# Kernel optimization log

Measured on AMD Instinct MI355X. Metric: run time of the kernel, lower is better.

Reference implementation:

```python
import jax, jax.numpy as jnp
import numpy as np

HIDDEN_DIM = 64
VOCAB_SIZE = 64
NUM_SLOTS = 64
B, L = 256, 4096
EPS = 1e-5


def setup_inputs() -> dict:
    key = jax.random.key(0)
    ks = jax.random.split(key, 8)
    s = 0.02
    return {
        "seq": jax.random.randint(ks[0], (B, L), 0, VOCAB_SIZE),
        "embed": jax.random.normal(ks[1], (VOCAB_SIZE, HIDDEN_DIM), jnp.float32) * s,
        "W1": jax.random.normal(ks[2], (HIDDEN_DIM, 2 * HIDDEN_DIM), jnp.float32) * s,
        "b1": jnp.zeros((2 * HIDDEN_DIM,), jnp.float32),
        "W2": jax.random.normal(ks[3], (2 * HIDDEN_DIM, HIDDEN_DIM), jnp.float32) * s,
        "b2": jnp.zeros((HIDDEN_DIM,), jnp.float32),
        "gamma": jnp.ones((HIDDEN_DIM,), jnp.float32),
        "beta": jnp.zeros((HIDDEN_DIM,), jnp.float32),
        "Wq": jax.random.normal(ks[4], (HIDDEN_DIM, HIDDEN_DIM), jnp.float32) * s,
        "bq": jnp.zeros((HIDDEN_DIM,), jnp.float32),
        "Wo": jax.random.normal(ks[5], (HIDDEN_DIM, VOCAB_SIZE), jnp.float32) * s,
        "bo": jnp.zeros((VOCAB_SIZE,), jnp.float32),
    }


def reference(seq, embed, W1, b1, W2, b2, gamma, beta, Wq, bq, Wo, bo):
    # Encoder: embed -> FF residual -> LayerNorm
    e = embed[seq]                                   # [B, L, H]
    ff = jax.nn.relu(e @ W1 + b1) @ W2 + b2          # [B, L, H]
    h = e + ff
    mu = jnp.mean(h, axis=-1, keepdims=True)
    var = jnp.mean(jnp.square(h - mu), axis=-1, keepdims=True)
    hs = (h - mu) * jax.lax.rsqrt(var + EPS) * gamma + beta  # [B, L, H]

    # Top-k gating over content token norms
    content = hs[:, :-3, :]                          # [B, L-3, H]
    gate_scores = jnp.linalg.norm(content, axis=-1)  # [B, L-3]
    _, idx = jax.lax.top_k(gate_scores, NUM_SLOTS)   # [B, k], k == num_slots (L-3 >= k)
    slots = jnp.take_along_axis(content, idx[:, :, None], axis=1)  # [B, k, H]

    # Tiny single-query attention over gathered slots
    q = hs[:, -1, :] @ Wq + bq                       # [B, H]
    scores = jnp.einsum("bh,bkh->bk", q, slots) / jnp.sqrt(jnp.float32(HIDDEN_DIM))
    attn = jax.nn.softmax(scores, axis=-1)           # [B, k]
    ctx = jnp.einsum("bk,bkh->bh", attn, slots)      # [B, H]
    return ctx @ Wo + bo                             # [B, VOCAB]
```

## Files before the change

### kernel.cpp

```cpp
#include <hip/hip_runtime.h>
#include <math.h>

#define EPS 1e-5f


__global__ __launch_bounds__(256) void table_and_hist(
    const int* __restrict__ seq,
    const float* __restrict__ embed,
    const float* __restrict__ W1, const float* __restrict__ b1,
    const float* __restrict__ W2, const float* __restrict__ b2,
    const float* __restrict__ gamma, const float* __restrict__ beta,
    float* __restrict__ wsf, int* __restrict__ wsi_hist,
    int* __restrict__ wsi_tlast)
{
    const int tid = threadIdx.x;

    if (blockIdx.x < 64) {
        __shared__ float W1s[64][128];
        __shared__ float W2s[128][64];
        __shared__ float e[64];
        __shared__ float Up[2][128];
        __shared__ float U[128];
        __shared__ float Hp[4][64];

        const int t = blockIdx.x;

        #pragma unroll
        for (int i = 0; i < 8; ++i) {
            reinterpret_cast<float4*>(&W1s[0][0])[tid + 256 * i] =
                reinterpret_cast<const float4*>(W1)[tid + 256 * i];
            reinterpret_cast<float4*>(&W2s[0][0])[tid + 256 * i] =
                reinterpret_cast<const float4*>(W2)[tid + 256 * i];
        }
        if (tid < 64) e[tid] = embed[t * 64 + tid];
        __syncthreads();

        {
            int j = tid & 127, h = tid >> 7;
            int k0 = h << 5;
            float acc = 0.f;
            #pragma unroll 8
            for (int k = 0; k < 32; ++k)
                acc = fmaf(e[k0 + k], W1s[k0 + k][j], acc);
            Up[h][j] = acc;
        }
        __syncthreads();
        if (tid < 128) U[tid] = fmaxf(b1[tid] + Up[0][tid] + Up[1][tid], 0.f);
        __syncthreads();

        {
            int j = tid & 63, qd = tid >> 6;
            int k0 = qd << 5;
            float acc = 0.f;
            #pragma unroll 8
            for (int k = 0; k < 32; ++k)
                acc = fmaf(U[k0 + k], W2s[k0 + k][j], acc);
            Hp[qd][j] = acc;
        }
        __syncthreads();

        if (tid < 64) {
            float h = e[tid] + b2[tid] + Hp[0][tid] + Hp[1][tid] + Hp[2][tid] + Hp[3][tid];
            float s = h;
            #pragma unroll
            for (int off = 1; off < 64; off <<= 1) s += __shfl_xor(s, off);
            float mu = s * (1.f / 64.f);
            float d = h - mu;
            float v = d * d;
            #pragma unroll
            for (int off = 1; off < 64; off <<= 1) v += __shfl_xor(v, off);
            float rstd = rsqrtf(v * (1.f / 64.f) + EPS);
            float hs = d * rstd * gamma[tid] + beta[tid];
            wsf[t * 64 + tid] = hs;
            float ss = hs * hs;
            #pragma unroll
            for (int off = 1; off < 64; off <<= 1) ss += __shfl_xor(ss, off);
            if (tid == 0) wsf[4096 + t] = sqrtf(ss);
        }
    } else {
        __shared__ int hist[4][64];
        const int b = blockIdx.x - 64;
        const int wv = tid >> 6, ln = tid & 63;
        const int* row = seq + b * 4096;

        hist[wv][ln] = 0;
        __syncthreads();

        #pragma unroll
        for (int i = 0; i < 4; ++i) {
            int idx = tid + 256 * i;
            if (idx < 1023) {
                int4 v = reinterpret_cast<const int4*>(row)[idx];
                atomicAdd(&hist[wv][v.x], 1);
                atomicAdd(&hist[wv][v.y], 1);
                atomicAdd(&hist[wv][v.z], 1);
                atomicAdd(&hist[wv][v.w], 1);
            }
        }
        if (tid == 0) {
            atomicAdd(&hist[0][row[4092]], 1);
            wsi_tlast[b] = row[4095];
        }
        __syncthreads();

        if (tid < 64)
            wsi_hist[b * 64 + tid] =
                hist[0][tid] + hist[1][tid] + hist[2][tid] + hist[3][tid];
    }
}

__global__ __launch_bounds__(256) void slot_epilogue(
    const float* __restrict__ Wq, const float* __restrict__ bq,
    const float* __restrict__ Wo, const float* __restrict__ bo,
    const float* __restrict__ wsf, const int* __restrict__ wsi_hist,
    const int* __restrict__ wsi_tlast,
    float* __restrict__ out)
{
    __shared__ float HS[64][65];
    __shared__ float qv[64];

    const int tid = threadIdx.x;
    const int wv  = tid >> 6;
    const int ln  = tid & 63;
    const int b   = blockIdx.x;

    float wcol[64];
    float bias = 0.f, sc_r = 0.f;
    int h = 0, tl = 0;
    if (wv == 0) {
        #pragma unroll
        for (int k = 0; k < 64; ++k) wcol[k] = Wo[k * 64 + ln];
        bias = bo[ln];
        sc_r = wsf[4096 + ln];
        h    = wsi_hist[b * 64 + ln];
    } else if (wv == 1) {
        #pragma unroll
        for (int k = 0; k < 64; ++k) wcol[k] = Wq[k * 64 + ln];
        bias = bq[ln];
        tl   = wsi_tlast[b];
    }

    #pragma unroll
    for (int i = 0; i < 4; ++i) {
        int idx4 = tid + 256 * i;
        float4 v = reinterpret_cast<const float4*>(wsf)[idx4];
        int t  = idx4 >> 4;
        int j0 = (idx4 & 15) << 2;
        HS[t][j0] = v.x; HS[t][j0+1] = v.y; HS[t][j0+2] = v.z; HS[t][j0+3] = v.w;
    }
    __syncthreads();

    int cnt_i = 0;
    if (wv == 0) {
        float my = sc_r;
        int S = 0;
        for (int t2 = 0; t2 < 64; ++t2) {
            float s2 = __shfl(sc_r, t2);
            int   h2 = __shfl(h, t2);
            bool before = (s2 > my) || (s2 == my && t2 < ln);
            if (before) S += h2;
        }
        int rem = 64 - S;
        rem = rem < 0 ? 0 : rem;
        cnt_i = h < rem ? h : rem;
    } else if (wv == 1) {
        float acc = bias;
        #pragma unroll
        for (int k = 0; k < 64; ++k)
            acc = fmaf(HS[tl][k], wcol[k], acc);
        qv[ln] = acc;
    }
    __syncthreads();

    if (wv == 0) {
        float acc = 0.f;
        #pragma unroll 8
        for (int k = 0; k < 64; ++k)
            acc = fmaf(qv[k], HS[ln][k], acc);
        float logit = acc * 0.125f;
        float lm = (cnt_i > 0) ? logit : -1e30f;
        #pragma unroll
        for (int off = 1; off < 64; off <<= 1) lm = fmaxf(lm, __shfl_xor(lm, off));
        float wvv = (cnt_i > 0) ? (float)cnt_i * __expf(logit - lm) : 0.f;
        float z = wvv;
        #pragma unroll
        for (int off = 1; off < 64; off <<= 1) z += __shfl_xor(z, off);
        float w_reg = wvv / z;

        float cacc = 0.f;
        #pragma unroll 8
        for (int t2 = 0; t2 < 64; ++t2)
            cacc = fmaf(__shfl(w_reg, t2), HS[t2][ln], cacc);

        float oacc = bias;
        #pragma unroll
        for (int k = 0; k < 64; ++k)
            oacc = fmaf(__shfl(cacc, k), wcol[k], oacc);
        out[b * 64 + ln] = oacc;
    }
}

extern "C" void kernel_launch(void* const* d_in, const int* in_sizes, int n_in,
                              void* d_out, int out_size, void* d_ws, size_t ws_size,
                              hipStream_t stream) {
    const int*   seq   = (const int*)d_in[0];
    const float* embed = (const float*)d_in[1];
    const float* W1    = (const float*)d_in[2];
    const float* b1    = (const float*)d_in[3];
    const float* W2    = (const float*)d_in[4];
    const float* b2    = (const float*)d_in[5];
    const float* gamma = (const float*)d_in[6];
    const float* beta  = (const float*)d_in[7];
    const float* Wq    = (const float*)d_in[8];
    const float* bq    = (const float*)d_in[9];
    const float* Wo    = (const float*)d_in[10];
    const float* bo    = (const float*)d_in[11];
    float* out = (float*)d_out;
    float* wsf = (float*)d_ws;
    int*   wsi_hist  = (int*)(wsf + 4160);
    int*   wsi_tlast = wsi_hist + 256 * 64;
    (void)in_sizes; (void)n_in; (void)out_size; (void)ws_size;

    table_and_hist<<<320, 256, 0, stream>>>(seq, embed, W1, b1, W2, b2,
                                            gamma, beta, wsf, wsi_hist, wsi_tlast);
    slot_epilogue<<<256, 256, 0, stream>>>(Wq, bq, Wo, bo, wsf, wsi_hist,
                                           wsi_tlast, out);
}
```

Baseline: 16.94 us.

## Compute embedding table per wavefront with shuffles and widen histogram blocks

The encoder table is now computed one token per wavefront, eight tokens per 512-thread block. Each block reads W1/W2 straight from global memory and broadcasts activations with shuffles, where before every block staged both weight matrices into shared memory. The histogram blocks grow to 512 threads, issue both int4 loads before the barrier, and handle the tail token without a serial thread-0 path. The goal is to drop the large shared-memory staging and its barriers, at the cost of repeated global or L2 weight reads in the table blocks.

```diff
diff --git a/kernel.cpp b/kernel.cpp
--- a/kernel.cpp
+++ b/kernel.cpp
@@ -4,7 +4,7 @@
 #define EPS 1e-5f
 
 
-__global__ __launch_bounds__(256) void table_and_hist(
+__global__ __launch_bounds__(512) void table_hist(
     const int* __restrict__ seq,
     const float* __restrict__ embed,
     const float* __restrict__ W1, const float* __restrict__ b1,
@@ -14,98 +14,83 @@
     int* __restrict__ wsi_tlast)
 {
     const int tid = threadIdx.x;
-
-    if (blockIdx.x < 64) {
-        __shared__ float W1s[64][128];
-        __shared__ float W2s[128][64];
-        __shared__ float e[64];
-        __shared__ float Up[2][128];
-        __shared__ float U[128];
-        __shared__ float Hp[4][64];
-
-        const int t = blockIdx.x;
-
-        #pragma unroll
-        for (int i = 0; i < 8; ++i) {
-            reinterpret_cast<float4*>(&W1s[0][0])[tid + 256 * i] =
-                reinterpret_cast<const float4*>(W1)[tid + 256 * i];
-            reinterpret_cast<float4*>(&W2s[0][0])[tid + 256 * i] =
-                reinterpret_cast<const float4*>(W2)[tid + 256 * i];
-        }
-        if (tid < 64) e[tid] = embed[t * 64 + tid];
+    const int wv  = tid >> 6;
+    const int ln  = tid & 63;
+
+    if (blockIdx.x < 8) {
+        const int t = blockIdx.x * 8 + wv;
+        float e = embed[t * 64 + ln];
+
+        float a0p0 = b1[ln],      a0p1 = 0.f;
+        float a1p0 = b1[64 + ln], a1p1 = 0.f;
+        #pragma unroll 8
+        for (int j = 0; j < 64; j += 2) {
+            float ej0 = __shfl(e, j);
+            float ej1 = __shfl(e, j + 1);
+            a0p0 = fmaf(ej0, W1[j * 128 + ln],            a0p0);
+            a1p0 = fmaf(ej0, W1[j * 128 + 64 + ln],       a1p0);
+            a0p1 = fmaf(ej1, (W1 + 128)[j * 128 + ln],      a0p1);
+            a1p1 = fmaf(ej1, (W1 + 128)[j * 128 + 64 + ln], a1p1);
+        }
+        float u0 = fmaxf(a0p0 + a0p1, 0.f);
+        float u1 = fmaxf(a1p0 + a1p1, 0.f);
+
+        float hp0 = e + b2[ln], hp1 = 0.f;
+        #pragma unroll 8
+        for (int k = 0; k < 64; k += 2) {
+            hp0 = fmaf(__shfl(u0, k),     W2[k * 64 + ln],       hp0);
+            hp1 = fmaf(__shfl(u0, k + 1), W2[(k + 1) * 64 + ln], hp1);
+        }
+        #pragma unroll 8
+        for (int k = 0; k < 64; k += 2) {
+            hp0 = fmaf(__shfl(u1, k),     W2[(64 + k) * 64 + ln],     hp0);
+            hp1 = fmaf(__shfl(u1, k + 1), W2[(64 + k + 1) * 64 + ln], hp1);
+        }
+        float h = hp0 + hp1;
+
+        float s = h;
+        #pragma unroll
+        for (int off = 1; off < 64; off <<= 1) s += __shfl_xor(s, off);
+        float mu = s * (1.f / 64.f);
+        float d = h - mu;
+        float v = d * d;
+        #pragma unroll
+        for (int off = 1; off < 64; off <<= 1) v += __shfl_xor(v, off);
+        float rstd = rsqrtf(v * (1.f / 64.f) + EPS);
+        float hs = d * rstd * gamma[ln] + beta[ln];
+        wsf[t * 64 + ln] = hs;
+        float ss = hs * hs;
+        #pragma unroll
+        for (int off = 1; off < 64; off <<= 1) ss += __shfl_xor(ss, off);
+        if (ln == 0) wsf[4096 + t] = sqrtf(ss);
+    } else {
+        __shared__ int hist[8][64];
+        const int b = blockIdx.x - 8;
+        const int* row = seq + b * 4096;
+
+        hist[wv][ln] = 0;
+        int4 v0 = reinterpret_cast<const int4*>(row)[tid];
+        int4 v1 = reinterpret_cast<const int4*>(row)[tid + 512];
         __syncthreads();
 
-        {
-            int j = tid & 127, h = tid >> 7;
-            int k0 = h << 5;
-            float acc = 0.f;
-            #pragma unroll 8
-            for (int k = 0; k < 32; ++k)
-                acc = fmaf(e[k0 + k], W1s[k0 + k][j], acc);
-            Up[h][j] = acc;
+        atomicAdd(&hist[wv][v0.x], 1); atomicAdd(&hist[wv][v0.y], 1);
+        atomicAdd(&hist[wv][v0.z], 1); atomicAdd(&hist[wv][v0.w], 1);
+        atomicAdd(&hist[wv][v1.x], 1);
+        if (tid != 511) {
+            atomicAdd(&hist[wv][v1.y], 1);
+            atomicAdd(&hist[wv][v1.z], 1);
+            atomicAdd(&hist[wv][v1.w], 1);
+        } else {
+            wsi_tlast[b] = v1.w;
         }
         __syncthreads();
-        if (tid < 128) U[tid] = fmaxf(b1[tid] + Up[0][tid] + Up[1][tid], 0.f);
-        __syncthreads();
-
-        {
-            int j = tid & 63, qd = tid >> 6;
-            int k0 = qd << 5;
-            float acc = 0.f;
-            #pragma unroll 8
-            for (int k = 0; k < 32; ++k)
-                acc = fmaf(U[k0 + k], W2s[k0 + k][j], acc);
-            Hp[qd][j] = acc;
-        }
-        __syncthreads();
 
         if (tid < 64) {
-            float h = e[tid] + b2[tid] + Hp[0][tid] + Hp[1][tid] + Hp[2][tid] + Hp[3][tid];
-            float s = h;
+            int hsum = 0;
             #pragma unroll
-            for (int off = 1; off < 64; off <<= 1) s += __shfl_xor(s, off);
-            float mu = s * (1.f / 64.f);
-            float d = h - mu;
-            float v = d * d;
-            #pragma unroll
-            for (int off = 1; off < 64; off <<= 1) v += __shfl_xor(v, off);
-            float rstd = rsqrtf(v * (1.f / 64.f) + EPS);
-            float hs = d * rstd * gamma[tid] + beta[tid];
-            wsf[t * 64 + tid] = hs;
-            float ss = hs * hs;
-            #pragma unroll
-            for (int off = 1; off < 64; off <<= 1) ss += __shfl_xor(ss, off);
-            if (tid == 0) wsf[4096 + t] = sqrtf(ss);
-        }
-    } else {
-        __shared__ int hist[4][64];
-        const int b = blockIdx.x - 64;
-        const int wv = tid >> 6, ln = tid & 63;
-        const int* row = seq + b * 4096;
-
-        hist[wv][ln] = 0;
-        __syncthreads();
-
-        #pragma unroll
-        for (int i = 0; i < 4; ++i) {
-            int idx = tid + 256 * i;
-            if (idx < 1023) {
-                int4 v = reinterpret_cast<const int4*>(row)[idx];
-                atomicAdd(&hist[wv][v.x], 1);
-                atomicAdd(&hist[wv][v.y], 1);
-                atomicAdd(&hist[wv][v.z], 1);
-                atomicAdd(&hist[wv][v.w], 1);
-            }
-        }
-        if (tid == 0) {
-            atomicAdd(&hist[0][row[4092]], 1);
-            wsi_tlast[b] = row[4095];
-        }
-        __syncthreads();
-
-        if (tid < 64)
-            wsi_hist[b * 64 + tid] =
-                hist[0][tid] + hist[1][tid] + hist[2][tid] + hist[3][tid];
+            for (int w = 0; w < 8; ++w) hsum += hist[w][tid];
+            wsi_hist[b * 64 + tid] = hsum;
+        }
     }
 }
 
@@ -144,8 +129,7 @@
     for (int i = 0; i < 4; ++i) {
         int idx4 = tid + 256 * i;
         float4 v = reinterpret_cast<const float4*>(wsf)[idx4];
-        int t  = idx4 >> 4;
-        int j0 = (idx4 & 15) << 2;
+        int t = idx4 >> 4, j0 = (idx4 & 15) << 2;
         HS[t][j0] = v.x; HS[t][j0+1] = v.y; HS[t][j0+2] = v.z; HS[t][j0+3] = v.w;
     }
     __syncthreads();
@@ -221,8 +205,8 @@
     int*   wsi_tlast = wsi_hist + 256 * 64;
     (void)in_sizes; (void)n_in; (void)out_size; (void)ws_size;
 
-    table_and_hist<<<320, 256, 0, stream>>>(seq, embed, W1, b1, W2, b2,
-                                            gamma, beta, wsf, wsi_hist, wsi_tlast);
+    table_hist<<<264, 512, 0, stream>>>(seq, embed, W1, b1, W2, b2,
+                                        gamma, beta, wsf, wsi_hist, wsi_tlast);
     slot_epilogue<<<256, 256, 0, stream>>>(Wq, bq, Wo, bo, wsf, wsi_hist,
                                            wsi_tlast, out);
 }
```

After: 19.82 us. 1.17x slower.
